# Performance work log

Measured on AMD Instinct MI355X. Metric: run time of the kernel, lower is better.

The kernel has to match this reference:

```python
import jax, jax.numpy as jnp
import numpy as np

IMG_SIZE = 256
NUM_ANGLES = 360
NUM_DET = 363  # ceil(sqrt(2) * IMG_SIZE)


def setup_inputs() -> dict:
    key = jax.random.key(0)
    sinogram = jax.random.normal(key, (2, 1, NUM_ANGLES, NUM_DET), dtype=jnp.float32)
    return {"sinogram": sinogram}


def _fbp(sinogram):
    B, C, A, D = sinogram.shape
    H = W = IMG_SIZE

    # ---- ramp filter in frequency domain (filter_type='ramp') ----
    freq = jnp.fft.fftfreq(D).astype(jnp.float32)          # (D,)
    filt = 2.0 * jnp.abs(freq)
    sino_fft = jnp.fft.fft(sinogram, axis=-1)
    filtered = jnp.fft.ifft(sino_fft * filt, axis=-1).real.astype(sinogram.dtype)  # (B,C,A,D)

    # ---- backprojection geometry ----
    angles = jnp.linspace(0.0, np.pi * (1.0 - 1.0 / A), A).astype(jnp.float32)  # (A,)
    coords = jnp.linspace(-1.0, 1.0, H).astype(jnp.float32)
    y_grid, x_grid = jnp.meshgrid(coords, coords, indexing='ij')  # (H,W) each

    cos_t = jnp.cos(angles)[:, None, None]  # (A,1,1)
    sin_t = jnp.sin(angles)[:, None, None]
    t = x_grid[None] * cos_t + y_grid[None] * sin_t          # (A,H,W)

    scale = (H - 1) / 2.0 * np.sqrt(2.0) / ((D - 1) / 2.0)
    t_norm = t / scale                                        # normalized grid x in [-1,1]-ish

    # grid_sample, mode='bilinear', padding_mode='zeros', align_corners=True
    # x-coordinate maps to detector index: u = (t_norm + 1)/2 * (D-1)
    u = (t_norm + 1.0) * 0.5 * (D - 1)                        # (A,H,W)
    u0 = jnp.floor(u)
    w1 = u - u0                                               # frac weight for right neighbor
    w0 = 1.0 - w1
    i0 = u0.astype(jnp.int32)
    i1 = i0 + 1
    valid0 = ((i0 >= 0) & (i0 < D)).astype(sinogram.dtype)
    valid1 = ((i1 >= 0) & (i1 < D)).astype(sinogram.dtype)
    i0c = jnp.clip(i0, 0, D - 1)
    i1c = jnp.clip(i1, 0, D - 1)

    HW = H * W
    idx0 = jnp.broadcast_to(i0c.reshape(1, 1, A, HW), (B, C, A, HW))
    idx1 = jnp.broadcast_to(i1c.reshape(1, 1, A, HW), (B, C, A, HW))
    v0 = jnp.take_along_axis(filtered, idx0, axis=-1)         # (B,C,A,HW)
    v1 = jnp.take_along_axis(filtered, idx1, axis=-1)

    w0m = (w0 * valid0).reshape(1, 1, A, HW)
    w1m = (w1 * valid1).reshape(1, 1, A, HW)
    contrib = v0 * w0m + v1 * w1m                             # (B,C,A,HW)

    recon = contrib.sum(axis=2).reshape(B, C, H, W)
    return recon * (np.pi / A)


def reference(sinogram):
    return _fbp(sinogram)
```

## Files before the change

### kernel.cpp

```cpp
#include <hip/hip_runtime.h>
#include <math.h>

#define IMG 256
#define NA  360
#define ND  363
#define NB  2
#define KMAX 181
#define ST  544
#define PAD 76

__global__ __launch_bounds__(384) void fbp_conv(const float* __restrict__ sino,
                                                float* __restrict__ filt) {
    __shared__ float ht[2 * ND - 1];
    const int row = blockIdx.x;
    const int t = threadIdx.x;

    for (int i = t; i < 2 * ND - 1; i += 384) {
        int n = i - (ND - 1);
        double S;
        if (n == 0) {
            S = (double)KMAX * (double)(KMAX + 1) * 0.5;
        } else {
            double w = (2.0 * M_PI / (double)ND) * (double)n;
            S = ((double)(KMAX + 1) * cos((double)KMAX * w)
               - (double)KMAX * cos((double)(KMAX + 1) * w) - 1.0)
              / (2.0 * (1.0 - cos(w)));
        }
        ht[i] = (float)(S * (4.0 / ((double)ND * (double)ND)));
    }
    __syncthreads();

    const float* __restrict__ srow = sino + (size_t)row * ND;
    float* __restrict__ orow = filt + (size_t)row * ST;

    if (t < ND) {
        float acc = 0.f;
#pragma unroll 4
        for (int m = ND - 1; m >= 0; --m) {
            acc = fmaf(srow[m], ht[t + (ND - 1) - m], acc);
        }
        orow[PAD + t] = acc;
    }
    if (t < PAD) orow[t] = 0.f;
    if (t >= PAD && t < PAD + (ST - PAD - ND)) orow[PAD + ND + (t - PAD)] = 0.f;
}

__global__ __launch_bounds__(256, 8) void fbp_backproj(const float* __restrict__ filt,
                                                       float* __restrict__ out,
                                                       float K, float U0p) {
    __shared__ float2 tab[NA];
    __shared__ float  part[256];
    const int t = threadIdx.x;
    for (int a = t; a < NA; a += 256) {
        float ang = (float)M_PI * (float)a / (float)NA;
        float s, c;
        sincosf(ang, &s, &c);
        tab[a] = make_float2(c * K, s * K);
    }
    __syncthreads();

    const int blk  = blockIdx.x;
    const int img  = blk >> 10;
    const int iy   = (blk >> 2) & 255;
    const int jx0  = (blk & 3) * 64;
    const int lane = t & 63;
    const int wv   = t >> 6;

    const float xg = -1.f + 2.f * (float)(jx0 + lane) / 255.f;
    const float yg = -1.f + 2.f * (float)iy / 255.f;

    const float* __restrict__ base = filt + (size_t)img * NA * ST;
    float acc = 0.f;
    const int a0 = wv * (NA / 4);

#pragma unroll 6
    for (int a = a0; a < a0 + NA / 4; ++a) {
        float2 cs = tab[a];
        float u  = fmaf(xg, cs.x, fmaf(yg, cs.y, U0p));
        float uf = floorf(u);
        int   i0 = (int)uf;
        float w  = u - uf;
        const float* rowp = base + a * ST;
        float2 tp = *(const float2*)(rowp + i0);
        acc = fmaf(w, tp.y - tp.x, acc + tp.x);
    }

    part[t] = acc;
    __syncthreads();

    if (t < 64) {
        float s = part[t] + part[t + 64] + part[t + 128] + part[t + 192];
        out[img * 65536 + iy * 256 + jx0 + t] = s * ((float)M_PI / (float)NA);
    }
}

extern "C" void kernel_launch(void* const* d_in, const int* in_sizes, int n_in,
                              void* d_out, int out_size, void* d_ws, size_t ws_size,
                              hipStream_t stream) {
    const float* sino = (const float*)d_in[0];
    float* out = (float*)d_out;
    float* filt = (float*)d_ws;

    const double scale = (double)(IMG - 1) / 2.0 * sqrt(2.0) / ((double)(ND - 1) / 2.0);
    const float  K   = (float)(0.5 * (double)(ND - 1) / scale);
    const float  U0p = 0.5f * (float)(ND - 1) + (float)PAD;

    fbp_conv<<<NB * NA, 384, 0, stream>>>(sino, filt);
    fbp_backproj<<<2048, 256, 0, stream>>>(filt, out, K, U0p);
}
```

Measured before the change: 95.69 us.

## Precompute ramp kernel once and register-block convolution four outputs per thread

The ramp-filter impulse response, previously recomputed in double precision by every conv block into shared memory, is now built once by a separate tiny kernel into global workspace. The convolution kernel then has each of 91 threads compute four adjacent outputs, loading the filter as float4 from global and reusing each sinogram sample across four FMAs. This removes redundant double-precision trig work and the per-block barrier, but adds an extra kernel launch and relies on cached global loads for the filter table.

```diff
diff --git a/kernel.cpp b/kernel.cpp
--- a/kernel.cpp
+++ b/kernel.cpp
@@ -8,15 +8,14 @@
 #define KMAX 181
 #define ST  544
 #define PAD 76
+#define HT_N 736
 
-__global__ __launch_bounds__(384) void fbp_conv(const float* __restrict__ sino,
-                                                float* __restrict__ filt) {
-    __shared__ float ht[2 * ND - 1];
-    const int row = blockIdx.x;
-    const int t = threadIdx.x;
-
-    for (int i = t; i < 2 * ND - 1; i += 384) {
-        int n = i - (ND - 1);
+__global__ void fbp_ht(float* __restrict__ ht) {
+    int i = blockIdx.x * 368 + threadIdx.x;
+    if (i >= HT_N) return;
+    float v = 0.f;
+    if (i <= 724) {
+        int n = i - 362;
         double S;
         if (n == 0) {
             S = (double)KMAX * (double)(KMAX + 1) * 0.5;
@@ -26,23 +25,61 @@
                - (double)KMAX * cos((double)(KMAX + 1) * w) - 1.0)
               / (2.0 * (1.0 - cos(w)));
         }
-        ht[i] = (float)(S * (4.0 / ((double)ND * (double)ND)));
+        v = (float)(S * (4.0 / ((double)ND * (double)ND)));
     }
-    __syncthreads();
+    ht[i] = v;
+}
 
+__global__ __launch_bounds__(128) void fbp_conv(const float* __restrict__ sino,
+                                                const float* __restrict__ htg,
+                                                float* __restrict__ filt) {
+    const int row = blockIdx.x;
+    const int t = threadIdx.x;
     const float* __restrict__ srow = sino + (size_t)row * ND;
     float* __restrict__ orow = filt + (size_t)row * ST;
+    const float4* __restrict__ ht4 = (const float4*)htg;
 
-    if (t < ND) {
-        float acc = 0.f;
-#pragma unroll 4
-        for (int m = ND - 1; m >= 0; --m) {
-            acc = fmaf(srow[m], ht[t + (ND - 1) - m], acc);
+    if (t < 91) {
+        float acc0 = 0.f, acc1 = 0.f, acc2 = 0.f, acc3 = 0.f;
+
+#pragma unroll 2
+        for (int c = 0; c < 45; ++c) {
+            float4 A = ht4[t + 2 * c];
+            float4 B = ht4[t + 2 * c + 1];
+            float4 C = ht4[t + 2 * c + 2];
+            const float W[12] = {A.x, A.y, A.z, A.w, B.x, B.y, B.z, B.w,
+                                 C.x, C.y, C.z, C.w};
+            const int m0 = 362 - 8 * c;
+#pragma unroll
+            for (int j = 0; j < 8; ++j) {
+                float s = srow[m0 - j];
+                acc0 = fmaf(s, W[j + 0], acc0);
+                acc1 = fmaf(s, W[j + 1], acc1);
+                acc2 = fmaf(s, W[j + 2], acc2);
+                acc3 = fmaf(s, W[j + 3], acc3);
+            }
         }
-        orow[PAD + t] = acc;
+        {
+            float4 A = ht4[t + 90];
+            float4 B = ht4[t + 91];
+            const float W[8] = {A.x, A.y, A.z, A.w, B.x, B.y, B.z, B.w};
+#pragma unroll
+            for (int j = 0; j < 3; ++j) {
+                float s = srow[2 - j];
+                acc0 = fmaf(s, W[j + 0], acc0);
+                acc1 = fmaf(s, W[j + 1], acc1);
+                acc2 = fmaf(s, W[j + 2], acc2);
+                acc3 = fmaf(s, W[j + 3], acc3);
+            }
+        }
+        const int d0 = 4 * t;
+        orow[PAD + d0 + 0] = acc0;
+        if (d0 + 1 < ND) orow[PAD + d0 + 1] = acc1;
+        if (d0 + 2 < ND) orow[PAD + d0 + 2] = acc2;
+        if (d0 + 3 < ND) orow[PAD + d0 + 3] = acc3;
     }
-    if (t < PAD) orow[t] = 0.f;
-    if (t >= PAD && t < PAD + (ST - PAD - ND)) orow[PAD + ND + (t - PAD)] = 0.f;
+    for (int i = t; i < PAD; i += 128) orow[i] = 0.f;
+    for (int i = t; i < ST - (PAD + ND); i += 128) orow[PAD + ND + i] = 0.f;
 }
 
 __global__ __launch_bounds__(256, 8) void fbp_backproj(const float* __restrict__ filt,
@@ -99,12 +136,14 @@
                               hipStream_t stream) {
     const float* sino = (const float*)d_in[0];
     float* out = (float*)d_out;
-    float* filt = (float*)d_ws;
+    float* htg  = (float*)d_ws;
+    float* filt = (float*)d_ws + 768;
 
     const double scale = (double)(IMG - 1) / 2.0 * sqrt(2.0) / ((double)(ND - 1) / 2.0);
     const float  K   = (float)(0.5 * (double)(ND - 1) / scale);
     const float  U0p = 0.5f * (float)(ND - 1) + (float)PAD;
 
-    fbp_conv<<<NB * NA, 384, 0, stream>>>(sino, filt);
+    fbp_ht<<<2, 368, 0, stream>>>(htg);
+    fbp_conv<<<NB * NA, 128, 0, stream>>>(sino, htg, filt);
     fbp_backproj<<<2048, 256, 0, stream>>>(filt, out, K, U0p);
 }
```

After: 92.15 us. -3.7%, faster.
